# Kernel tuning notes

Hardware: AMD Instinct MI355X
Metric: run time of the kernel (lower is better)

Reference implementation:

```python
import jax, jax.numpy as jnp
import numpy as np

D_MODEL = 512
D_FFN = 4 * D_MODEL
EPS = 1e-5


def layer_norm(x, gamma, beta):
    mu = jnp.mean(x, axis=-1, keepdims=True)
    var = jnp.mean(jnp.square(x - mu), axis=-1, keepdims=True)
    return (x - mu) * jax.lax.rsqrt(var + EPS) * gamma + beta


def setup_inputs() -> dict:
    key = jax.random.key(0)
    ks = jax.random.split(key, 12)
    B, S, D, F = 4, 2048, D_MODEL, D_FFN
    s = 1.0 / np.sqrt(D)
    inp = {
        "q": jax.random.normal(ks[0], (B, S, D), jnp.float32),
        "k": jax.random.normal(ks[1], (B, S, D), jnp.float32),
        "v": jax.random.normal(ks[2], (B, S, D), jnp.float32),
        "x": jax.random.normal(ks[3], (B, S, D), jnp.float32),
        "Wq": jax.random.normal(ks[4], (D, D), jnp.float32) * s,
        "bq": jnp.zeros((D,), jnp.float32),
        "Wk": jax.random.normal(ks[5], (D, D), jnp.float32) * s,
        "bk": jnp.zeros((D,), jnp.float32),
        "Wv": jax.random.normal(ks[6], (D, D), jnp.float32) * s,
        "bv": jnp.zeros((D,), jnp.float32),
        "g1": jnp.ones((D,), jnp.float32),
        "be1": jnp.zeros((D,), jnp.float32),
        "W1": jax.random.normal(ks[7], (D, F), jnp.float32) * s,
        "b1": jnp.zeros((F,), jnp.float32),
        "W2": jax.random.normal(ks[8], (F, D), jnp.float32) * (1.0 / np.sqrt(F)),
        "b2": jnp.zeros((D,), jnp.float32),
        "g2": jnp.ones((D,), jnp.float32),
        "be2": jnp.zeros((D,), jnp.float32),
    }
    return inp


def reference(q, k, v, x, Wq, bq, Wk, bk, Wv, bv, g1, be1, W1, b1, W2, b2, g2, be2):
    # QKV projections: [B,S,D] @ [D,D]
    Q = jnp.einsum("bsd,de->bse", q, Wq) + bq
    K = jnp.einsum("bsd,de->bse", k, Wk) + bk
    V = jnp.einsum("bsd,de->bse", v, Wv) + bv
    d_k = Q.shape[-1]
    # scaled dot-product attention, full [B,S,S] scores as in the original
    scores = jnp.einsum("bqd,bkd->bqk", Q, K) / jnp.sqrt(jnp.float32(d_k))
    probs = jax.nn.softmax(scores, axis=-1)
    attn = jnp.einsum("bqk,bkd->bqd", probs, V)
    # residual + LayerNorm
    h = layer_norm(attn + x, g1, be1)
    # position-wise FFN
    f = jnp.maximum(jnp.einsum("bsd,df->bsf", h, W1) + b1, 0.0)
    f = jnp.einsum("bsf,fd->bsd", f, W2) + b2
    # residual + LayerNorm
    return layer_norm(f + h, g2, be2)
```

## Files before the change

### kernel.cpp

```cpp
#include <hip/hip_runtime.h>


typedef __attribute__((ext_vector_type(8))) short short8;
typedef __attribute__((ext_vector_type(4))) float f32x4;

__device__ __forceinline__ unsigned short f2bf(float f) {
    unsigned int u = __float_as_uint(f);
    unsigned int r = (u + 0x7FFFu + ((u >> 16) & 1u)) >> 16;
    return (unsigned short)r;
}

__device__ __forceinline__ void gload_lds16(const void* g, void* l) {
    __builtin_amdgcn_global_load_lds(
        (const __attribute__((address_space(1))) void*)g,
        (__attribute__((address_space(3))) void*)l, 16, 0, 0);
}

__global__ __launch_bounds__(256) void cast_f32_bf16(
    const float* __restrict__ in, unsigned short* __restrict__ out, long n4) {
    long i = (long)blockIdx.x * blockDim.x + threadIdx.x;
    if (i < n4) {
        float4 v = ((const float4*)in)[i];
        ushort4 o;
        o.x = f2bf(v.x); o.y = f2bf(v.y); o.z = f2bf(v.z); o.w = f2bf(v.w);
        ((ushort4*)out)[i] = o;
    }
}

__global__ __launch_bounds__(256) void transpose_cast_f32_bf16(
    const float* __restrict__ in, unsigned short* __restrict__ out, int R, int C) {
    __shared__ float t[32][33];
    int c0 = blockIdx.x * 32, r0 = blockIdx.y * 32;
    int x = threadIdx.x;
    for (int i = threadIdx.y; i < 32; i += 8)
        t[i][x] = in[(long)(r0 + i) * C + c0 + x];
    __syncthreads();
    for (int i = threadIdx.y; i < 32; i += 8)
        out[(long)(c0 + i) * R + r0 + x] = f2bf(t[x][i]);
}

__global__ __launch_bounds__(256) void transpose_bf16(
    const unsigned short* __restrict__ in, unsigned short* __restrict__ out,
    int R, int C, long inBatch, long outBatch) {
    __shared__ unsigned short t[32][33];
    long z = blockIdx.z;
    in += z * inBatch; out += z * outBatch;
    int c0 = blockIdx.x * 32, r0 = blockIdx.y * 32;
    int x = threadIdx.x;
    for (int i = threadIdx.y; i < 32; i += 8)
        t[i][x] = in[(long)(r0 + i) * C + c0 + x];
    __syncthreads();
    for (int i = threadIdx.y; i < 32; i += 8)
        out[(long)(c0 + i) * R + r0 + x] = t[x][i];
}

template<int BIAS, int RELU, int OUT_BF16>
__global__ __launch_bounds__(256, 2) void gemm_nt(
    const unsigned short* __restrict__ A, const unsigned short* __restrict__ BT,
    const float* __restrict__ bias, void* __restrict__ C,
    int M, int N, int K, long aBatch, long bBatch, long cBatch) {
    __shared__ __align__(16) unsigned short As[4096];
    __shared__ __align__(16) unsigned short Bs[4096];
    const int tid  = threadIdx.x;
    const int wave = tid >> 6;
    const int lane = tid & 63;
    const long z = blockIdx.z;
    A  += z * aBatch;
    BT += z * bBatch;
    const int row0 = blockIdx.y * 128;
    const int col0 = blockIdx.x * 128;
    const int wr = (wave >> 1) * 64;
    const int wc = (wave & 1) * 64;

    f32x4 acc[4][4] = {};

    const unsigned short* Ag = A  + (long)(row0 + (tid >> 2)) * K + (tid & 3) * 8;
    const unsigned short* Bg = BT + (long)(col0 + (tid >> 2)) * K + (tid & 3) * 8;
    unsigned short* AsBase = &As[wave * 512];
    unsigned short* BsBase = &Bs[wave * 512];

    const int lr  = lane & 15;
    const int kq8 = (lane >> 4) * 8;

    for (int k0 = 0; k0 < K; k0 += 32) {
        __syncthreads();
        #pragma unroll
        for (int c = 0; c < 2; ++c) {
            gload_lds16(Ag + (long)c * 64 * K + k0, AsBase + c * 2048);
            gload_lds16(Bg + (long)c * 64 * K + k0, BsBase + c * 2048);
        }
        __syncthreads();

        short8 af[4], bf[4];
        #pragma unroll
        for (int m = 0; m < 4; ++m)
            af[m] = *(const short8*)&As[(wr + m * 16 + lr) * 32 + kq8];
        #pragma unroll
        for (int n = 0; n < 4; ++n)
            bf[n] = *(const short8*)&Bs[(wc + n * 16 + lr) * 32 + kq8];
        #pragma unroll
        for (int m = 0; m < 4; ++m)
            #pragma unroll
            for (int n = 0; n < 4; ++n)
                acc[m][n] = __builtin_amdgcn_mfma_f32_16x16x32_bf16(
                    af[m], bf[n], acc[m][n], 0, 0, 0);
    }

    const int orow = row0 + wr + (lane >> 4) * 4;
    const int ocol = col0 + wc + lr;
    const long cb = z * cBatch;
    #pragma unroll
    for (int n = 0; n < 4; ++n) {
        const int cc = ocol + n * 16;
        float bv = 0.0f;
        if (BIAS) bv = bias[cc];
        #pragma unroll
        for (int m = 0; m < 4; ++m) {
            #pragma unroll
            for (int j = 0; j < 4; ++j) {
                float v = acc[m][n][j] + bv;
                if (RELU) v = fmaxf(v, 0.0f);
                long off = cb + (long)(orow + m * 16 + j) * N + cc;
                if (OUT_BF16) ((unsigned short*)C)[off] = f2bf(v);
                else          ((float*)C)[off] = v;
            }
        }
    }
}

__global__ __launch_bounds__(256) void softmax_rows(
    const float* __restrict__ S, unsigned short* __restrict__ P, float scale) {
    long row = blockIdx.x;
    const float4* src = (const float4*)(S + row * 2048);
    int tid = threadIdx.x;
    int wave = tid >> 6, lane = tid & 63;
    float4 a = src[tid], b = src[tid + 256];
    float e[8] = { a.x * scale, a.y * scale, a.z * scale, a.w * scale,
                   b.x * scale, b.y * scale, b.z * scale, b.w * scale };
    float m = e[0];
    #pragma unroll
    for (int i = 1; i < 8; ++i) m = fmaxf(m, e[i]);
    #pragma unroll
    for (int o = 32; o > 0; o >>= 1) m = fmaxf(m, __shfl_xor(m, o));
    __shared__ float redm[4], reds[4];
    if (lane == 0) redm[wave] = m;
    __syncthreads();
    m = fmaxf(fmaxf(redm[0], redm[1]), fmaxf(redm[2], redm[3]));
    float s = 0.0f;
    #pragma unroll
    for (int i = 0; i < 8; ++i) { e[i] = __expf(e[i] - m); s += e[i]; }
    #pragma unroll
    for (int o = 32; o > 0; o >>= 1) s += __shfl_xor(s, o);
    if (lane == 0) reds[wave] = s;
    __syncthreads();
    s = reds[0] + reds[1] + reds[2] + reds[3];
    float inv = 1.0f / s;
    ushort4 o0, o1;
    o0.x = f2bf(e[0] * inv); o0.y = f2bf(e[1] * inv);
    o0.z = f2bf(e[2] * inv); o0.w = f2bf(e[3] * inv);
    o1.x = f2bf(e[4] * inv); o1.y = f2bf(e[5] * inv);
    o1.z = f2bf(e[6] * inv); o1.w = f2bf(e[7] * inv);
    ushort4* dst = (ushort4*)(P + row * 2048);
    dst[tid] = o0;
    dst[tid + 256] = o1;
}

template<int DUAL>
__global__ __launch_bounds__(128) void ln_kernel(
    const float* __restrict__ A, const float* __restrict__ R,
    const float* __restrict__ g, const float* __restrict__ be,
    float* __restrict__ out, unsigned short* __restrict__ outbf) {
    long row = blockIdx.x;
    int tid = threadIdx.x;
    int wave = tid >> 6, lane = tid & 63;
    float4 va = ((const float4*)(A + row * 512))[tid];
    float4 vr = ((const float4*)(R + row * 512))[tid];
    float4 v;
    v.x = va.x + vr.x; v.y = va.y + vr.y; v.z = va.z + vr.z; v.w = va.w + vr.w;
    float s  = v.x + v.y + v.z + v.w;
    float s2 = v.x * v.x + v.y * v.y + v.z * v.z + v.w * v.w;
    #pragma unroll
    for (int o = 32; o > 0; o >>= 1) { s += __shfl_xor(s, o); s2 += __shfl_xor(s2, o); }
    __shared__ float r1[2], r2[2];
    if (lane == 0) { r1[wave] = s; r2[wave] = s2; }
    __syncthreads();
    s = r1[0] + r1[1]; s2 = r2[0] + r2[1];
    float mu = s * (1.0f / 512.0f);
    float var = s2 * (1.0f / 512.0f) - mu * mu;
    float rs = rsqrtf(var + 1e-5f);
    float4 gg = ((const float4*)g)[tid];
    float4 bb = ((const float4*)be)[tid];
    float4 y;
    y.x = (v.x - mu) * rs * gg.x + bb.x;
    y.y = (v.y - mu) * rs * gg.y + bb.y;
    y.z = (v.z - mu) * rs * gg.z + bb.z;
    y.w = (v.w - mu) * rs * gg.w + bb.w;
    ((float4*)(out + row * 512))[tid] = y;
    if (DUAL) {
        ushort4 o;
        o.x = f2bf(y.x); o.y = f2bf(y.y); o.z = f2bf(y.z); o.w = f2bf(y.w);
        ((ushort4*)(outbf + row * 512))[tid] = o;
    }
}

extern "C" void kernel_launch(void* const* d_in, const int* in_sizes, int n_in,
                              void* d_out, int out_size, void* d_ws, size_t ws_size,
                              hipStream_t stream) {
    const float* q   = (const float*)d_in[0];
    const float* k   = (const float*)d_in[1];
    const float* v   = (const float*)d_in[2];
    const float* x   = (const float*)d_in[3];
    const float* Wq  = (const float*)d_in[4];
    const float* bq  = (const float*)d_in[5];
    const float* Wk  = (const float*)d_in[6];
    const float* bk  = (const float*)d_in[7];
    const float* Wv  = (const float*)d_in[8];
    const float* bv  = (const float*)d_in[9];
    const float* g1  = (const float*)d_in[10];
    const float* be1 = (const float*)d_in[11];
    const float* W1  = (const float*)d_in[12];
    const float* b1  = (const float*)d_in[13];
    const float* W2  = (const float*)d_in[14];
    const float* b2  = (const float*)d_in[15];
    const float* g2  = (const float*)d_in[16];
    const float* be2 = (const float*)d_in[17];
    float* out = (float*)d_out;

    const int B = 4, S = 2048, D = 512, F = 2048;
    const long BS = (long)B * S;
    const long SD = (long)S * D;
    const long SS = (long)S * S;

    char* ws = (char*)d_ws;
    size_t off = 0;
    auto alloc = [&](size_t bytes) -> void* {
        void* p = ws + off;
        off += (bytes + 255) & ~(size_t)255;
        return p;
    };
    unsigned short* WqT = (unsigned short*)alloc((size_t)D * D * 2);
    unsigned short* WkT = (unsigned short*)alloc((size_t)D * D * 2);
    unsigned short* WvT = (unsigned short*)alloc((size_t)D * D * 2);
    unsigned short* W1T = (unsigned short*)alloc((size_t)D * F * 2);
    unsigned short* W2T = (unsigned short*)alloc((size_t)F * D * 2);
    unsigned short* qb = (unsigned short*)alloc(BS * D * 2);
    unsigned short* kb = (unsigned short*)alloc(BS * D * 2);
    unsigned short* vb = (unsigned short*)alloc(BS * D * 2);
    float* attn = (float*)qb;
    unsigned short* Qb = (unsigned short*)alloc(BS * D * 2);
    unsigned short* Kb = (unsigned short*)alloc(BS * D * 2);
    unsigned short* Vb = (unsigned short*)alloc(BS * D * 2);
    float* h_f32 = (float*)Qb;
    unsigned short* h_bf = Vb;
    unsigned short* VT = (unsigned short*)alloc(BS * D * 2);
    float* Sc = (float*)alloc((size_t)B * SS * 4);
    unsigned short* f_bf = (unsigned short*)Sc;
    float* f2 = (float*)((char*)Sc + (size_t)BS * F * 2);
    unsigned short* Pb = (unsigned short*)alloc((size_t)B * SS * 2);

    const float scale = 0.04419417382415922f;

    {
        long n4 = BS * D / 4;
        int blocks = (int)((n4 + 255) / 256);
        cast_f32_bf16<<<blocks, 256, 0, stream>>>(q, qb, n4);
        cast_f32_bf16<<<blocks, 256, 0, stream>>>(k, kb, n4);
        cast_f32_bf16<<<blocks, 256, 0, stream>>>(v, vb, n4);
    }
    transpose_cast_f32_bf16<<<dim3(D/32, D/32), dim3(32, 8), 0, stream>>>(Wq, WqT, D, D);
    transpose_cast_f32_bf16<<<dim3(D/32, D/32), dim3(32, 8), 0, stream>>>(Wk, WkT, D, D);
    transpose_cast_f32_bf16<<<dim3(D/32, D/32), dim3(32, 8), 0, stream>>>(Wv, WvT, D, D);
    transpose_cast_f32_bf16<<<dim3(F/32, D/32), dim3(32, 8), 0, stream>>>(W1, W1T, D, F);
    transpose_cast_f32_bf16<<<dim3(D/32, F/32), dim3(32, 8), 0, stream>>>(W2, W2T, F, D);
    gemm_nt<1,0,1><<<dim3(D/128, BS/128, 1), 256, 0, stream>>>(qb, WqT, bq, Qb, (int)BS, D, D, 0, 0, 0);
    gemm_nt<1,0,1><<<dim3(D/128, BS/128, 1), 256, 0, stream>>>(kb, WkT, bk, Kb, (int)BS, D, D, 0, 0, 0);
    gemm_nt<1,0,1><<<dim3(D/128, BS/128, 1), 256, 0, stream>>>(vb, WvT, bv, Vb, (int)BS, D, D, 0, 0, 0);
    transpose_bf16<<<dim3(D/32, S/32, B), dim3(32, 8), 0, stream>>>(Vb, VT, S, D, SD, SD);
    gemm_nt<0,0,0><<<dim3(S/128, S/128, B), 256, 0, stream>>>(Qb, Kb, nullptr, Sc, S, S, D, SD, SD, SS);
    softmax_rows<<<(int)BS, 256, 0, stream>>>(Sc, Pb, scale);
    gemm_nt<0,0,0><<<dim3(D/128, S/128, B), 256, 0, stream>>>(Pb, VT, nullptr, attn, S, D, S, SS, SD, SD);
    ln_kernel<1><<<(int)BS, 128, 0, stream>>>(attn, x, g1, be1, h_f32, h_bf);
    gemm_nt<1,1,1><<<dim3(F/128, BS/128, 1), 256, 0, stream>>>(h_bf, W1T, b1, f_bf, (int)BS, F, D, 0, 0, 0);
    gemm_nt<1,0,0><<<dim3(D/128, BS/128, 1), 256, 0, stream>>>(f_bf, W2T, b2, f2, (int)BS, D, F, 0, 0, 0);
    ln_kernel<0><<<(int)BS, 128, 0, stream>>>(f2, h_f32, g2, be2, out, nullptr);
}
```

Measured before the change: 382.7 us.

## Double-buffer GEMM LDS tiles and fold softmax scale into score GEMM

The GEMM kernel now uses two LDS buffers and prefetches the next K tile with global_load_lds while MFMAs run on the current tile, dropping one barrier per iteration. The attention scale moves from the softmax kernel into the score GEMM epilogue. Explicit leading-dimension parameters are added. LDS usage doubles, which could affect occupancy, and correctness relies on the barrier waiting for the async LDS loads.

```diff
diff --git a/kernel.cpp b/kernel.cpp
--- a/kernel.cpp
+++ b/kernel.cpp
@@ -41,14 +41,14 @@
 
 __global__ __launch_bounds__(256) void transpose_bf16(
     const unsigned short* __restrict__ in, unsigned short* __restrict__ out,
-    int R, int C, long inBatch, long outBatch) {
+    int R, int C, int inLd, long inBatch, long outBatch) {
     __shared__ unsigned short t[32][33];
     long z = blockIdx.z;
     in += z * inBatch; out += z * outBatch;
     int c0 = blockIdx.x * 32, r0 = blockIdx.y * 32;
     int x = threadIdx.x;
     for (int i = threadIdx.y; i < 32; i += 8)
-        t[i][x] = in[(long)(r0 + i) * C + c0 + x];
+        t[i][x] = in[(long)(r0 + i) * inLd + c0 + x];
     __syncthreads();
     for (int i = threadIdx.y; i < 32; i += 8)
         out[(long)(c0 + i) * R + r0 + x] = t[x][i];
@@ -58,9 +58,10 @@
 __global__ __launch_bounds__(256, 2) void gemm_nt(
     const unsigned short* __restrict__ A, const unsigned short* __restrict__ BT,
     const float* __restrict__ bias, void* __restrict__ C,
-    int M, int N, int K, long aBatch, long bBatch, long cBatch) {
-    __shared__ __align__(16) unsigned short As[4096];
-    __shared__ __align__(16) unsigned short Bs[4096];
+    int N, int K, int lda, int ldb, int ldc,
+    long aBatch, long bBatch, long cBatch, float scale) {
+    __shared__ __align__(16) unsigned short As[2][4096];
+    __shared__ __align__(16) unsigned short Bs[2][4096];
     const int tid  = threadIdx.x;
     const int wave = tid >> 6;
     const int lane = tid & 63;
@@ -74,36 +75,45 @@
 
     f32x4 acc[4][4] = {};
 
-    const unsigned short* Ag = A  + (long)(row0 + (tid >> 2)) * K + (tid & 3) * 8;
-    const unsigned short* Bg = BT + (long)(col0 + (tid >> 2)) * K + (tid & 3) * 8;
-    unsigned short* AsBase = &As[wave * 512];
-    unsigned short* BsBase = &Bs[wave * 512];
+    const unsigned short* Ag = A  + (long)(row0 + (tid >> 2)) * lda + (tid & 3) * 8;
+    const unsigned short* Bg = BT + (long)(col0 + (tid >> 2)) * ldb + (tid & 3) * 8;
+    const int sBase = wave * 512;
 
     const int lr  = lane & 15;
     const int kq8 = (lane >> 4) * 8;
-
-    for (int k0 = 0; k0 < K; k0 += 32) {
-        __syncthreads();
-        #pragma unroll
-        for (int c = 0; c < 2; ++c) {
-            gload_lds16(Ag + (long)c * 64 * K + k0, AsBase + c * 2048);
-            gload_lds16(Bg + (long)c * 64 * K + k0, BsBase + c * 2048);
+    const int nk = K >> 5;
+
+    #pragma unroll
+    for (int c = 0; c < 2; ++c) {
+        gload_lds16(Ag + (long)c * 64 * lda, &As[0][sBase + c * 2048]);
+        gload_lds16(Bg + (long)c * 64 * ldb, &Bs[0][sBase + c * 2048]);
+    }
+    __syncthreads();
+
+    for (int t = 0; t < nk; ++t) {
+        const int cur = t & 1;
+        if (t + 1 < nk) {
+            const int k0 = (t + 1) << 5;
+            #pragma unroll
+            for (int c = 0; c < 2; ++c) {
+                gload_lds16(Ag + (long)c * 64 * lda + k0, &As[cur ^ 1][sBase + c * 2048]);
+                gload_lds16(Bg + (long)c * 64 * ldb + k0, &Bs[cur ^ 1][sBase + c * 2048]);
+            }
         }
-        __syncthreads();
-
         short8 af[4], bf[4];
         #pragma unroll
         for (int m = 0; m < 4; ++m)
-            af[m] = *(const short8*)&As[(wr + m * 16 + lr) * 32 + kq8];
+            af[m] = *(const short8*)&As[cur][(wr + m * 16 + lr) * 32 + kq8];
         #pragma unroll
         for (int n = 0; n < 4; ++n)
-            bf[n] = *(const short8*)&Bs[(wc + n * 16 + lr) * 32 + kq8];
+            bf[n] = *(const short8*)&Bs[cur][(wc + n * 16 + lr) * 32 + kq8];
         #pragma unroll
         for (int m = 0; m < 4; ++m)
             #pragma unroll
             for (int n = 0; n < 4; ++n)
                 acc[m][n] = __builtin_amdgcn_mfma_f32_16x16x32_bf16(
                     af[m], bf[n], acc[m][n], 0, 0, 0);
+        __syncthreads();
     }
 
     const int orow = row0 + wr + (lane >> 4) * 4;
@@ -118,9 +128,9 @@
         for (int m = 0; m < 4; ++m) {
             #pragma unroll
             for (int j = 0; j < 4; ++j) {
-                float v = acc[m][n][j] + bv;
+                float v = acc[m][n][j] * scale + bv;
                 if (RELU) v = fmaxf(v, 0.0f);
-                long off = cb + (long)(orow + m * 16 + j) * N + cc;
+                long off = cb + (long)(orow + m * 16 + j) * ldc + cc;
                 if (OUT_BF16) ((unsigned short*)C)[off] = f2bf(v);
                 else          ((float*)C)[off] = v;
             }
@@ -129,14 +139,13 @@
 }
 
 __global__ __launch_bounds__(256) void softmax_rows(
-    const float* __restrict__ S, unsigned short* __restrict__ P, float scale) {
+    const float* __restrict__ S, unsigned short* __restrict__ P) {
     long row = blockIdx.x;
     const float4* src = (const float4*)(S + row * 2048);
     int tid = threadIdx.x;
     int wave = tid >> 6, lane = tid & 63;
     float4 a = src[tid], b = src[tid + 256];
-    float e[8] = { a.x * scale, a.y * scale, a.z * scale, a.w * scale,
-                   b.x * scale, b.y * scale, b.z * scale, b.w * scale };
+    float e[8] = { a.x, a.y, a.z, a.w, b.x, b.y, b.z, b.w };
     float m = e[0];
     #pragma unroll
     for (int i = 1; i < 8; ++i) m = fmaxf(m, e[i]);
@@ -272,15 +281,15 @@
     transpose_cast_f32_bf16<<<dim3(D/32, D/32), dim3(32, 8), 0, stream>>>(Wv, WvT, D, D);
     transpose_cast_f32_bf16<<<dim3(F/32, D/32), dim3(32, 8), 0, stream>>>(W1, W1T, D, F);
     transpose_cast_f32_bf16<<<dim3(D/32, F/32), dim3(32, 8), 0, stream>>>(W2, W2T, F, D);
-    gemm_nt<1,0,1><<<dim3(D/128, BS/128, 1), 256, 0, stream>>>(qb, WqT, bq, Qb, (int)BS, D, D, 0, 0, 0);
-    gemm_nt<1,0,1><<<dim3(D/128, BS/128, 1), 256, 0, stream>>>(kb, WkT, bk, Kb, (int)BS, D, D, 0, 0, 0);
-    gemm_nt<1,0,1><<<dim3(D/128, BS/128, 1), 256, 0, stream>>>(vb, WvT, bv, Vb, (int)BS, D, D, 0, 0, 0);
-    transpose_bf16<<<dim3(D/32, S/32, B), dim3(32, 8), 0, stream>>>(Vb, VT, S, D, SD, SD);
-    gemm_nt<0,0,0><<<dim3(S/128, S/128, B), 256, 0, stream>>>(Qb, Kb, nullptr, Sc, S, S, D, SD, SD, SS);
-    softmax_rows<<<(int)BS, 256, 0, stream>>>(Sc, Pb, scale);
-    gemm_nt<0,0,0><<<dim3(D/128, S/128, B), 256, 0, stream>>>(Pb, VT, nullptr, attn, S, D, S, SS, SD, SD);
+    gemm_nt<1,0,1><<<dim3(D/128, BS/128, 1), 256, 0, stream>>>(qb, WqT, bq, Qb, D, D, D, D, D, 0, 0, 0, 1.0f);
+    gemm_nt<1,0,1><<<dim3(D/128, BS/128, 1), 256, 0, stream>>>(kb, WkT, bk, Kb, D, D, D, D, D, 0, 0, 0, 1.0f);
+    gemm_nt<1,0,1><<<dim3(D/128, BS/128, 1), 256, 0, stream>>>(vb, WvT, bv, Vb, D, D, D, D, D, 0, 0, 0, 1.0f);
+    transpose_bf16<<<dim3(D/32, S/32, B), dim3(32, 8), 0, stream>>>(Vb, VT, S, D, D, SD, SD);
+    gemm_nt<0,0,0><<<dim3(S/128, S/128, B), 256, 0, stream>>>(Qb, Kb, nullptr, Sc, S, D, D, D, S, SD, SD, SS, scale);
+    softmax_rows<<<(int)BS, 256, 0, stream>>>(Sc, Pb);
+    gemm_nt<0,0,0><<<dim3(D/128, S/128, B), 256, 0, stream>>>(Pb, VT, nullptr, attn, D, S, S, S, D, SS, SD, SD, 1.0f);
     ln_kernel<1><<<(int)BS, 128, 0, stream>>>(attn, x, g1, be1, h_f32, h_bf);
-    gemm_nt<1,1,1><<<dim3(F/128, BS/128, 1), 256, 0, stream>>>(h_bf, W1T, b1, f_bf, (int)BS, F, D, 0, 0, 0);
-    gemm_nt<1,0,0><<<dim3(D/128, BS/128, 1), 256, 0, stream>>>(f_bf, W2T, b2, f2, (int)BS, D, F, 0, 0, 0);
+    gemm_nt<1,1,1><<<dim3(F/128, BS/128, 1), 256, 0, stream>>>(h_bf, W1T, b1, f_bf, F, D, D, D, F, 0, 0, 0, 1.0f);
+    gemm_nt<1,0,0><<<dim3(D/128, BS/128, 1), 256, 0, stream>>>(f_bf, W2T, b2, f2, D, F, F, F, D, 0, 0, 0, 1.0f);
     ln_kernel<0><<<(int)BS, 128, 0, stream>>>(f2, h_f32, g2, be2, out, nullptr);
 }
```

Result: no change. 386.1 us (+0.9%).
